# Kernel optimization log

Measured on AMD Instinct MI355X. Metric: run time of the kernel, lower is better.

Reference implementation:

```python
import jax, jax.numpy as jnp
import numpy as np

HEADS = 8
SCALE_BASE = 512
EPS = 1e-5


def xpos(x, downscale=False):
    # x: (B, h, S, hd) ; XPOS rotary embedding with exponential scale
    hd = x.shape[-1]
    S = x.shape[-2]
    half = hd // 2
    base_scale = (jnp.arange(0, hd, 2, dtype=jnp.float32) + 0.4 * hd) / (1.4 * hd)  # (half,)
    pos = jnp.arange(S, dtype=jnp.float32)
    scale = base_scale[None, :] ** (pos[:, None] / SCALE_BASE)  # (S, half)
    inv_freq = 1.0 / (10000.0 ** (jnp.arange(half, dtype=jnp.float32) / half))
    sinu = pos[:, None] * inv_freq[None, :]  # (S, half)
    sin, cos = jnp.sin(sinu), jnp.cos(sinu)
    if downscale:
        scale = 1.0 / scale
    # duplicate_interleave: (S, half) -> (S, hd)
    sin_s = jnp.repeat(sin * scale, 2, axis=-1)
    cos_s = jnp.repeat(cos * scale, 2, axis=-1)
    x1 = x[..., ::2]
    x2 = x[..., 1::2]
    rot = jnp.stack((-x2, x1), axis=-1).reshape(x.shape)  # rotate_every_two
    return x * cos_s + rot * sin_s


def decay_mask(S):
    # (heads, S, S): gamma^(n-m) for n>=m else 0
    gammas = 1.0 - jnp.exp(jnp.linspace(np.log(1 / 32), np.log(1 / 512), HEADS)).astype(jnp.float32)
    n = jnp.arange(S, dtype=jnp.float32)
    diff = n[:, None] - n[None, :]
    lg = jnp.log(gammas)[:, None, None]
    return jnp.where(diff >= 0, jnp.exp(jnp.maximum(diff, 0.0) * lg), 0.0)


def layer_norm(x, w, b):
    mu = x.mean(-1, keepdims=True)
    var = x.var(-1, keepdims=True)
    return (x - mu) / jnp.sqrt(var + EPS) * w + b


def multiscale_retention(Xq, Xkv, Wq, Wk, Wv, Wg, Wo, gn_w, gn_b):
    # Xq: (B,S,d) query source; Xkv: (B,S,d) key/value source (== Xq for self)
    B, S, _ = Xq.shape
    Q = jnp.einsum('bsd,hde->bhse', Xq, Wq)
    K = jnp.einsum('btd,hde->bhte', Xkv, Wk)
    V = jnp.einsum('btd,hdv->bhtv', Xkv, Wv)
    Q = xpos(Q)
    K = xpos(K, downscale=True)
    D = decay_mask(S)  # (h,S,S)
    scores = jnp.einsum('bhse,bhte->bhst', Q, K) * D[None]
    Y = jnp.einsum('bhst,bhtv->bhsv', scores, V)  # (B,h,S,hv)
    h, hv = Y.shape[1], Y.shape[3]
    # GroupNorm(heads, v_dim) over each head's channels per token
    mu = Y.mean(-1, keepdims=True)
    var = Y.var(-1, keepdims=True)
    Yn = (Y - mu) / jnp.sqrt(var + EPS)
    Yn = Yn.transpose(0, 2, 1, 3).reshape(B, S, h * hv) * gn_w + gn_b
    gate = jax.nn.sigmoid(Xq @ Wg) * (Xq @ Wg)  # swish gate
    return (gate * Yn) @ Wo


def setup_inputs() -> dict:
    key = jax.random.key(0)
    ks = jax.random.split(key, 32)
    d, f, h, hd, hv, vd = 1024, 4096, 8, 128, 256, 2048
    B, S = 2, 2048
    inp = {
        'X': jax.random.normal(ks[0], (B, S, d), jnp.float32),
        'mem': jax.random.normal(ks[1], (B, S, d), jnp.float32),
        'ln1_w': jax.random.uniform(ks[2], (d,), jnp.float32, 0.5, 1.5),
        'ln1_b': jax.random.normal(ks[3], (d,), jnp.float32) * 0.1,
        'ln2_w': jax.random.uniform(ks[4], (d,), jnp.float32, 0.5, 1.5),
        'ln2_b': jax.random.normal(ks[5], (d,), jnp.float32) * 0.1,
        'Wq': jax.random.normal(ks[6], (h, d, hd), jnp.float32) / d,
        'Wk': jax.random.normal(ks[7], (h, d, hd), jnp.float32) / d,
        'Wv': jax.random.normal(ks[8], (h, d, hv), jnp.float32) / d,
        'Wg': jax.random.normal(ks[9], (d, vd), jnp.float32) / d,
        'Wo': jax.random.normal(ks[10], (vd, d), jnp.float32) / d,
        'gn_w': jax.random.uniform(ks[11], (vd,), jnp.float32, 0.5, 1.5),
        'gn_b': jax.random.normal(ks[12], (vd,), jnp.float32) * 0.1,
        'cWq': jax.random.normal(ks[13], (h, d, hd), jnp.float32) / d,
        'cWk': jax.random.normal(ks[14], (h, d, hd), jnp.float32) / d,
        'cWv': jax.random.normal(ks[15], (h, d, hv), jnp.float32) / d,
        'cWg': jax.random.normal(ks[16], (d, vd), jnp.float32) / d,
        'cWo': jax.random.normal(ks[17], (vd, d), jnp.float32) / d,
        'cgn_w': jax.random.uniform(ks[18], (vd,), jnp.float32, 0.5, 1.5),
        'cgn_b': jax.random.normal(ks[19], (vd,), jnp.float32) * 0.1,
        'W1': jax.random.normal(ks[20], (d, f), jnp.float32) * (1.0 / np.sqrt(d)),
        'b1': jax.random.normal(ks[21], (f,), jnp.float32) * 0.02,
        'W2': jax.random.normal(ks[22], (f, d), jnp.float32) * (1.0 / np.sqrt(f)),
        'b2': jax.random.normal(ks[23], (d,), jnp.float32) * 0.02,
    }
    return inp


def reference(X, mem, ln1_w, ln1_b, ln2_w, ln2_b, Wq, Wk, Wv, Wg, Wo, gn_w, gn_b,
              cWq, cWk, cWv, cWg, cWo, cgn_w, cgn_b, W1, b1, W2, b2):
    # self retention block
    X = multiscale_retention(layer_norm(X, ln1_w, ln1_b), None, Wq, Wk, Wv, Wg, Wo, gn_w, gn_b) + X if False else multiscale_retention(layer_norm(X, ln1_w, ln1_b), layer_norm(X, ln1_w, ln1_b), Wq, Wk, Wv, Wg, Wo, gn_w, gn_b) + X
    # cross retention block (note: original reuses layer_norms_2 for both this and the FFN)
    h2 = layer_norm(X, ln2_w, ln2_b)
    X = multiscale_retention(h2, mem, cWq, cWk, cWv, cWg, cWo, cgn_w, cgn_b) + X
    # FFN block (GELU exact, per torch nn.GELU default)
    h3 = layer_norm(X, ln2_w, ln2_b)
    X = (jax.nn.gelu(h3 @ W1 + b1, approximate=False) @ W2 + b2) + X
    return X
```

## Files before the change

### kernel.cpp

```cpp
#include <hip/hip_runtime.h>
#include <math.h>

#define RTOT 4096
#define SEQQ 2048

typedef unsigned int uint32;
typedef __attribute__((ext_vector_type(4))) float f32x4;
typedef __attribute__((ext_vector_type(8))) short bf16x8;

__device__ __forceinline__ unsigned short f2bf(float f) {
  unsigned int u = __float_as_uint(f);
  u = (u + 0x7FFFu + ((u >> 16) & 1u)) >> 16;
  return (unsigned short)u;
}
__device__ __forceinline__ float bf2f(unsigned short h) {
  return __uint_as_float(((unsigned int)h) << 16);
}
__device__ __forceinline__ void gld16(const void* g, void* l) {
  __builtin_amdgcn_global_load_lds(
      (const __attribute__((address_space(1))) uint32*)g,
      (__attribute__((address_space(3))) uint32*)l, 16, 0, 0);
}
__device__ __forceinline__ void bar() {
  asm volatile("" ::: "memory");
  __builtin_amdgcn_s_barrier();
  asm volatile("" ::: "memory");
}
#define VMCNT(n) asm volatile("s_waitcnt vmcnt(" #n ")" ::: "memory")

__global__ __launch_bounds__(256) void transpose_bf16(
    const float* __restrict__ in, unsigned short* __restrict__ out, int R, int C,
    int perm) {
  __shared__ float t[32][33];
  int z = blockIdx.z;
  in  += (size_t)z * R * C;
  out += (size_t)z * C * R;
  int r0 = blockIdx.x * 32, c0 = blockIdx.y * 32;
  int tx = threadIdx.x & 31, ty = threadIdx.x >> 5;
  #pragma unroll
  for (int i = 0; i < 4; ++i) {
    int r = ty + i * 8;
    t[r][tx] = in[(size_t)(r0 + r) * C + c0 + tx];
  }
  __syncthreads();
  #pragma unroll
  for (int i = 0; i < 4; ++i) {
    int cc = c0 + ty + i * 8;
    if (perm) cc = 64 * (cc >> 6) + ((cc & 1) << 5) + ((cc & 63) >> 1);
    out[(size_t)cc * R + r0 + tx] = f2bf(t[tx][ty + i * 8]);
  }
}

__global__ __launch_bounds__(256) void cvt_bf16(
    const float* __restrict__ in, unsigned short* __restrict__ out, int n8) {
  int i = blockIdx.x * 256 + threadIdx.x;
  if (i >= n8) return;
  const float4* p = (const float4*)(in + (size_t)i * 8);
  float4 a = p[0], b = p[1];
  bf16x8 v;
  v[0] = (short)f2bf(a.x); v[1] = (short)f2bf(a.y); v[2] = (short)f2bf(a.z); v[3] = (short)f2bf(a.w);
  v[4] = (short)f2bf(b.x); v[5] = (short)f2bf(b.y); v[6] = (short)f2bf(b.z); v[7] = (short)f2bf(b.w);
  *(bf16x8*)(out + (size_t)i * 8) = v;
}

__global__ __launch_bounds__(256) void tabgen(float* __restrict__ tab) {
  int i = blockIdx.x * 256 + threadIdx.x;
  int pos = i >> 6, j = i & 63;
  float bs = (2.f * (float)j + 51.2f) * (1.f / 179.2f);
  float e = (float)pos * (1.f / 512.f);
  float sc = exp2f(e * log2f(bs));
  float invf = exp2f(-(float)j * (13.287712379549449f / 64.f));
  float su, cu;
  sincosf((float)pos * invf, &su, &cu);
  tab[i]            = cu * sc;
  tab[131072 + i]   = su * sc;
  float si = 1.f / sc;
  tab[262144 + i]   = cu * si;
  tab[393216 + i]   = su * si;
}

__global__ __launch_bounds__(256) void ln_bf16(const float* __restrict__ x,
    const float* __restrict__ w, const float* __restrict__ b,
    unsigned short* __restrict__ out) {
  int row = blockIdx.x, tid = threadIdx.x;
  const float* xr = x + (size_t)row * 1024;
  float4 v = *(const float4*)(xr + tid * 4);
  float s  = v.x + v.y + v.z + v.w;
  float ss = v.x*v.x + v.y*v.y + v.z*v.z + v.w*v.w;
  #pragma unroll
  for (int o = 32; o > 0; o >>= 1) { s += __shfl_down(s, o); ss += __shfl_down(ss, o); }
  __shared__ float red[2][4];
  int wid = tid >> 6;
  if ((tid & 63) == 0) { red[0][wid] = s; red[1][wid] = ss; }
  __syncthreads();
  float st  = red[0][0] + red[0][1] + red[0][2] + red[0][3];
  float sst = red[1][0] + red[1][1] + red[1][2] + red[1][3];
  float mu   = st * (1.f / 1024.f);
  float var  = sst * (1.f / 1024.f) - mu * mu;
  float rstd = rsqrtf(var + 1e-5f);
  float4 wv = *(const float4*)(w + tid * 4);
  float4 bv = *(const float4*)(b + tid * 4);
  unsigned short o0 = f2bf((v.x - mu) * rstd * wv.x + bv.x);
  unsigned short o1 = f2bf((v.y - mu) * rstd * wv.y + bv.y);
  unsigned short o2 = f2bf((v.z - mu) * rstd * wv.z + bv.z);
  unsigned short o3 = f2bf((v.w - mu) * rstd * wv.w + bv.w);
  ushort4 o4 = make_ushort4(o0, o1, o2, o3);
  *(ushort4*)(out + (size_t)row * 1024 + tid * 4) = o4;
}

enum { EPI_F32_RES = 0, EPI_BF16 = 1, EPI_XPOS = 2, EPI_GELU = 4, EPI_BRES = 5,
       EPI_QKG = 6, EPI_QG = 7 };

struct EpiP {
  void* C; int ldc;
  const float* bias; const float* resid;
  const float* tab;
  unsigned short* oQ; unsigned short* oK; unsigned short* oG;
};

template<int EPI>
__device__ __forceinline__ void epi_store(size_t m, int n, int N0, float v, const EpiP& P) {
  if constexpr (EPI == EPI_BF16) {
    ((unsigned short*)P.C)[m * P.ldc + n] = f2bf(v);
  } else if constexpr (EPI == EPI_GELU) {
    v += P.bias[n];
    v = 0.5f * v * (1.f + erff(v * 0.70710678f));
    ((unsigned short*)P.C)[m * P.ldc + n] = f2bf(v);
  } else if constexpr (EPI == EPI_BRES) {
    v += P.bias[n] + P.resid[m * P.ldc + n];
    ((float*)P.C)[m * P.ldc + n] = v;
  } else {
    v += P.resid[m * P.ldc + n];
    ((float*)P.C)[m * P.ldc + n] = v;
  }
}

template<int EPI>
__global__ __launch_bounds__(256) void gemm_mfma(
    const unsigned short* __restrict__ A, int lda,
    const unsigned short* __restrict__ Bt, int ldb, int K, EpiP P) {
  __shared__ __align__(16) unsigned short As[2][128 * 32];
  __shared__ __align__(16) unsigned short Bs[2][128 * 32];
  const int tid = threadIdx.x, w = tid >> 6, lane = tid & 63;
  const int M0 = blockIdx.y * 128, N0 = blockIdx.x * 128;
  const int fr = lane & 15, fs = lane >> 4;
  const int srow = lane >> 2, sp = lane & 3;

  f32x4 zf = {0.f, 0.f, 0.f, 0.f};
  f32x4 acc[4][4];
  #pragma unroll
  for (int i = 0; i < 4; ++i)
    #pragma unroll
    for (int j = 0; j < 4; ++j) acc[i][j] = zf;

  auto STAGE = [&](int buf, int k0) {
    #pragma unroll
    for (int c = 0; c < 4; ++c) {
      int ch = w * 4 + c;
      int cc = ch & 7;
      int row = cc * 16 + srow;
      int so = sp ^ ((row >> 1) & 3);
      if (ch < 8) gld16(A  + (size_t)(M0 + row) * lda + k0 + so * 8, &As[buf][cc * 512]);
      else        gld16(Bt + (size_t)(N0 + row) * ldb + k0 + so * 8, &Bs[buf][cc * 512]);
    }
  };

  STAGE(0, 0);
  int cur = 0;
  for (int k0 = 0; k0 < K; k0 += 32) {
    if (k0 + 32 < K) { STAGE(cur ^ 1, k0 + 32); VMCNT(4); }
    else             { VMCNT(0); }
    bar();
    bf16x8 af[4], bfr[4];
    #pragma unroll
    for (int mi = 0; mi < 4; ++mi) {
      int row = (w >> 1) * 64 + mi * 16 + fr;
      af[mi] = *(const bf16x8*)(&As[cur][row * 32 + (fs ^ ((row >> 1) & 3)) * 8]);
    }
    #pragma unroll
    for (int ni = 0; ni < 4; ++ni) {
      int row = (w & 1) * 64 + ni * 16 + fr;
      bfr[ni] = *(const bf16x8*)(&Bs[cur][row * 32 + (fs ^ ((row >> 1) & 3)) * 8]);
    }
    #pragma unroll
    for (int mi = 0; mi < 4; ++mi)
      #pragma unroll
      for (int ni = 0; ni < 4; ++ni)
        acc[mi][ni] = __builtin_amdgcn_mfma_f32_16x16x32_bf16(af[mi], bfr[ni], acc[mi][ni], 0, 0, 0);
    bar();
    cur ^= 1;
  }

  #pragma unroll
  for (int mi = 0; mi < 4; ++mi)
    #pragma unroll
    for (int r = 0; r < 4; ++r) {
      size_t m = M0 + (w >> 1) * 64 + mi * 16 + fs * 4 + r;
      #pragma unroll
      for (int ni = 0; ni < 4; ++ni) {
        int n = N0 + (w & 1) * 64 + ni * 16 + fr;
        epi_store<EPI>(m, n, N0, acc[mi][ni][r], P);
      }
    }
}

template<int EPI>
__global__ __launch_bounds__(256) void gemm_bn64(
    const unsigned short* __restrict__ A, int lda,
    const unsigned short* __restrict__ Bt, int ldb, int K, EpiP P) {
  __shared__ __align__(16) unsigned short As[2][128 * 32];
  __shared__ __align__(16) unsigned short Bs[2][64 * 32];
  const int tid = threadIdx.x, w = tid >> 6, lane = tid & 63;
  const int M0 = blockIdx.y * 128, N0 = blockIdx.x * 64;
  const int fr = lane & 15, fs = lane >> 4;
  const int srow = lane >> 2, sp = lane & 3;

  f32x4 zf = {0.f, 0.f, 0.f, 0.f};
  f32x4 acc[2][4];
  #pragma unroll
  for (int i = 0; i < 2; ++i)
    #pragma unroll
    for (int j = 0; j < 4; ++j) acc[i][j] = zf;

  auto STAGE = [&](int buf, int k0) {
    #pragma unroll
    for (int c = 0; c < 3; ++c) {
      int ch = w * 3 + c;
      if (ch < 8) {
        int row = ch * 16 + srow;
        int so = sp ^ ((row >> 1) & 3);
        gld16(A + (size_t)(M0 + row) * lda + k0 + so * 8, &As[buf][ch * 512]);
      } else {
        int bch = ch - 8;
        int row = bch * 16 + srow;
        int so = sp ^ ((row >> 1) & 3);
        gld16(Bt + (size_t)(N0 + row) * ldb + k0 + so * 8, &Bs[buf][bch * 512]);
      }
    }
  };

  STAGE(0, 0);
  int cur = 0;
  for (int k0 = 0; k0 < K; k0 += 32) {
    if (k0 + 32 < K) { STAGE(cur ^ 1, k0 + 32); VMCNT(3); }
    else             { VMCNT(0); }
    bar();
    bf16x8 af[2], bfr[4];
    #pragma unroll
    for (int mi = 0; mi < 2; ++mi) {
      int row = w * 32 + mi * 16 + fr;
      af[mi] = *(const bf16x8*)(&As[cur][row * 32 + (fs ^ ((row >> 1) & 3)) * 8]);
    }
    #pragma unroll
    for (int ni = 0; ni < 4; ++ni) {
      int row = ni * 16 + fr;
      bfr[ni] = *(const bf16x8*)(&Bs[cur][row * 32 + (fs ^ ((row >> 1) & 3)) * 8]);
    }
    #pragma unroll
    for (int mi = 0; mi < 2; ++mi)
      #pragma unroll
      for (int ni = 0; ni < 4; ++ni)
        acc[mi][ni] = __builtin_amdgcn_mfma_f32_16x16x32_bf16(af[mi], bfr[ni], acc[mi][ni], 0, 0, 0);
    bar();
    cur ^= 1;
  }

  if constexpr (EPI == EPI_XPOS) {
    int gsel = (N0 >> 6) & 1;
    #pragma unroll
    for (int mi = 0; mi < 2; ++mi)
      #pragma unroll
      for (int r = 0; r < 4; ++r) {
        size_t m = M0 + w * 32 + mi * 16 + fs * 4 + r;
        int pos = (int)(m & (SEQQ - 1));
        #pragma unroll
        for (int ni = 0; ni < 2; ++ni) {
          int j = gsel * 32 + ni * 16 + fr;
          float cs = P.tab[pos * 64 + j], sn = P.tab[131072 + pos * 64 + j];
          float ve = acc[mi][ni][r], vo = acc[mi][ni + 2][r];
          unsigned short* dst = (unsigned short*)P.C;
          dst[m * P.ldc + N0 + ni * 16 + fr]       = f2bf(ve * cs - vo * sn);
          dst[m * P.ldc + N0 + (ni + 2) * 16 + fr] = f2bf(vo * cs + ve * sn);
        }
      }
  } else {
    #pragma unroll
    for (int mi = 0; mi < 2; ++mi)
      #pragma unroll
      for (int r = 0; r < 4; ++r) {
        size_t m = M0 + w * 32 + mi * 16 + fs * 4 + r;
        #pragma unroll
        for (int ni = 0; ni < 4; ++ni) {
          int n = N0 + ni * 16 + fr;
          epi_store<EPI>(m, n, N0, acc[mi][ni][r], P);
        }
      }
  }
}

template<int EPI>
__global__ __launch_bounds__(512, 2) void gemm256(
    const unsigned short* __restrict__ A,
    const unsigned short* __restrict__ Bt,
    int nbx, EpiP P) {
  __shared__ __align__(16) unsigned short lds[4][2][8192];
  const int tid = threadIdx.x, w = tid >> 6, lane = tid & 63;
  int cpx = (int)gridDim.x >> 3;
  int sbid = ((int)blockIdx.x & 7) * cpx + ((int)blockIdx.x >> 3);
  int by = sbid / nbx, bx = sbid - by * nbx;
  const int M0 = by * 256, N0 = bx * 256;
  const int wm = w >> 2, wn = w & 3;
  const int fr = lane & 15, fs = lane >> 4;
  const int srow = lane >> 2;
  const int sslot = (lane & 3) ^ ((lane >> 3) & 3);
  const int rsw = (fr >> 1) & 3;

  f32x4 acc[8][4];
  #pragma unroll
  for (int i = 0; i < 8; ++i)
    #pragma unroll
    for (int j = 0; j < 4; ++j) acc[i][j] = {0.f, 0.f, 0.f, 0.f};

  auto STAGE = [&](int t, int buf) {
    int k0 = t * 32;
    #pragma unroll
    for (int j = 0; j < 4; ++j) {
      int c = w * 4 + j;
      if (c < 16)
        gld16(A  + (size_t)(M0 + c * 16 + srow) * 1024 + k0 + sslot * 8,
              &lds[buf][0][c * 512]);
      else
        gld16(Bt + (size_t)(N0 + (c - 16) * 16 + srow) * 1024 + k0 + sslot * 8,
              &lds[buf][1][(c - 16) * 512]);
    }
  };
  auto COMPUTE = [&](int t) {
    const unsigned short* la = &lds[t & 3][0][wm * 128 * 32];
    const unsigned short* lb = &lds[t & 3][1][wn * 64 * 32];
    bf16x8 a[8], b[4];
    #pragma unroll
    for (int ni = 0; ni < 4; ++ni)
      b[ni] = *(const bf16x8*)(lb + (ni * 16 + fr) * 32 + ((fs ^ rsw) * 8));
    #pragma unroll
    for (int mi = 0; mi < 8; ++mi)
      a[mi] = *(const bf16x8*)(la + (mi * 16 + fr) * 32 + ((fs ^ rsw) * 8));
    #pragma unroll
    for (int mi = 0; mi < 8; ++mi)
      #pragma unroll
      for (int ni = 0; ni < 4; ++ni)
        acc[mi][ni] = __builtin_amdgcn_mfma_f32_16x16x32_bf16(a[mi], b[ni], acc[mi][ni], 0, 0, 0);
  };

  STAGE(0, 0); STAGE(1, 1); STAGE(2, 2);
  for (int t = 0; t < 29; ++t) {
    STAGE(t + 3, (t + 3) & 3);
    VMCNT(12);
    bar();
    COMPUTE(t);
    bar();
  }
  VMCNT(8);  bar(); COMPUTE(29); bar();
  VMCNT(4);  bar(); COMPUTE(30); bar();
  VMCNT(0);  bar(); COMPUTE(31);

  if constexpr (EPI == EPI_GELU) {
    #pragma unroll
    for (int mi = 0; mi < 8; ++mi)
      #pragma unroll
      for (int r = 0; r < 4; ++r) {
        size_t m = M0 + wm * 128 + mi * 16 + fs * 4 + r;
        #pragma unroll
        for (int ni = 0; ni < 4; ++ni) {
          int n = N0 + wn * 64 + ni * 16 + fr;
          float v = acc[mi][ni][r] + P.bias[n];
          v = 0.5f * v * (1.f + erff(v * 0.70710678f));
          ((unsigned short*)P.C)[m * P.ldc + n] = f2bf(v);
        }
      }
  } else {
    const int nb = N0 + wn * 64;
    const bool isQ = nb < 1024;
    const bool isK = (EPI == EPI_QKG) && !isQ && (nb < 2048);
    if (isQ || isK) {
      const float* tc = isK ? P.tab + 262144 : P.tab;
      const float* ts = tc + 131072;
      unsigned short* dst = isK ? P.oK : P.oQ;
      const int nloc = isK ? nb - 1024 : nb;
      const int gsel = (nloc >> 6) & 1;
      #pragma unroll
      for (int mi = 0; mi < 8; ++mi)
        #pragma unroll
        for (int r = 0; r < 4; ++r) {
          size_t m = M0 + wm * 128 + mi * 16 + fs * 4 + r;
          int pos = (int)(m & (SEQQ - 1));
          #pragma unroll
          for (int ni = 0; ni < 2; ++ni) {
            int j = gsel * 32 + ni * 16 + fr;
            float cs = tc[pos * 64 + j], sn = ts[pos * 64 + j];
            float ve = acc[mi][ni][r], vo = acc[mi][ni + 2][r];
            dst[m * 1024 + nloc + ni * 16 + fr]       = f2bf(ve * cs - vo * sn);
            dst[m * 1024 + nloc + (ni + 2) * 16 + fr] = f2bf(vo * cs + ve * sn);
          }
        }
    } else {
      const int nloc = nb - ((EPI == EPI_QKG) ? 2048 : 1024);
      #pragma unroll
      for (int mi = 0; mi < 8; ++mi)
        #pragma unroll
        for (int r = 0; r < 4; ++r) {
          size_t m = M0 + wm * 128 + mi * 16 + fs * 4 + r;
          #pragma unroll
          for (int ni = 0; ni < 4; ++ni) {
            float v = acc[mi][ni][r];
            P.oG[m * 2048 + nloc + ni * 16 + fr] = f2bf(v / (1.f + expf(-v)));
          }
        }
    }
  }
}

__global__ __launch_bounds__(256) void retention_mfma(
    const unsigned short* __restrict__ Qx, const unsigned short* __restrict__ Kx,
    const unsigned short* __restrict__ VT, const unsigned short* __restrict__ Gate,
    const float* __restrict__ gnw, const float* __restrict__ gnb,
    unsigned short* __restrict__ Gout) {
  __shared__ __align__(16) unsigned short Ks[2][32 * 128];
  __shared__ __align__(16) unsigned short Vs[2][256 * 32];
  __shared__ __align__(16) float Ps[4][16 * 36];
  const int tid = threadIdx.x, w = tid >> 6, lane = tid & 63;
  int bid = blockIdx.x, qt, h, b;
  if (bid < 256) { qt = 31 - (bid >> 3); h = bid & 7; b = 0; }
  else           { int k = bid - 256; qt = k >> 3; h = k & 7; b = 1; }
  const int q0 = qt * 64;
  const int fr = lane & 15, fs = lane >> 4;

  float gamma = 1.f - expf(-3.4657359028f - 0.3960841032f * (float)h);
  float l2g = log2f(gamma);

  size_t qrow = (size_t)b * SEQQ + q0 + w * 16 + fr;
  bf16x8 qf[4];
  #pragma unroll
  for (int ks = 0; ks < 4; ++ks)
    qf[ks] = *(const bf16x8*)(Qx + qrow * 1024 + h * 128 + ks * 32 + fs * 8);

  float fqv[4];
  #pragma unroll
  for (int r = 0; r < 4; ++r)
    fqv[r] = exp2f((float)(q0 + w * 16 + fs * 4 + r) * l2g);

  f32x4 zf = {0.f, 0.f, 0.f, 0.f};
  f32x4 yacc[16];
  #pragma unroll
  for (int i = 0; i < 16; ++i) yacc[i] = zf;

  int cutoff = (int)(27.f / (-l2g));
  int t_start = q0 - cutoff;
  if (t_start < 0) t_start = 0;
  t_start &= ~31;
  size_t kbase = (size_t)b * SEQQ;

  auto STAGE = [&](int buf, int t0) {
    #pragma unroll
    for (int c = 0; c < 2; ++c) {
      int ch = w * 2 + c;
      int row = ch * 4 + (lane >> 4);
      int so = (lane & 15) ^ (row & 15);
      gld16(Kx + (kbase + t0 + row) * 1024 + h * 128 + so * 8, &Ks[buf][ch * 512]);
    }
    #pragma unroll
    for (int c = 0; c < 4; ++c) {
      int ch = w * 4 + c;
      int vrow = ch * 16 + (lane >> 2);
      int so = (lane & 3) ^ ((vrow >> 1) & 3);
      gld16(VT + (size_t)(h * 256 + vrow) * RTOT + kbase + t0 + so * 8, &Vs[buf][ch * 512]);
    }
  };

  STAGE(0, t_start);
  int cur = 0;
  for (int t0 = t_start; t0 < q0 + 64; t0 += 32) {
    if (t0 + 32 < q0 + 64) { STAGE(cur ^ 1, t0 + 32); VMCNT(6); }
    else                   { VMCNT(0); }
    bar();

    f32x4 sacc[2];
    sacc[0] = zf; sacc[1] = zf;
    #pragma unroll
    for (int nt = 0; nt < 2; ++nt) {
      int row = nt * 16 + fr;
      #pragma unroll
      for (int ks = 0; ks < 4; ++ks) {
        int sl = ks * 4 + fs;
        bf16x8 kf = *(const bf16x8*)(&Ks[cur][row * 128 + (sl ^ (row & 15)) * 8]);
        sacc[nt] = __builtin_amdgcn_mfma_f32_16x16x32_bf16(qf[ks], kf, sacc[nt], 0, 0, 0);
      }
    }
    float ftv[2];
    ftv[0] = exp2f((float)(t0 + fr)      * -l2g);
    ftv[1] = exp2f((float)(t0 + 16 + fr) * -l2g);
    float* Pw = Ps[w];
    #pragma unroll
    for (int nt = 0; nt < 2; ++nt) {
      #pragma unroll
      for (int r = 0; r < 4; ++r) {
        int sl_ = fs * 4 + r;
        int diff = (q0 + w * 16 + sl_) - (t0 + nt * 16 + fr);
        float v = (diff >= 0) ? sacc[nt][r] * (fqv[r] * ftv[nt]) : 0.f;
        Pw[sl_ * 36 + nt * 16 + fr] = v;
      }
    }
    f32x4 pa = *(const f32x4*)(Pw + fr * 36 + fs * 8);
    f32x4 pb = *(const f32x4*)(Pw + fr * 36 + fs * 8 + 4);
    bf16x8 pf;
    pf[0] = (short)f2bf(pa[0]); pf[1] = (short)f2bf(pa[1]);
    pf[2] = (short)f2bf(pa[2]); pf[3] = (short)f2bf(pa[3]);
    pf[4] = (short)f2bf(pb[0]); pf[5] = (short)f2bf(pb[1]);
    pf[6] = (short)f2bf(pb[2]); pf[7] = (short)f2bf(pb[3]);
    #pragma unroll
    for (int nv = 0; nv < 16; ++nv) {
      int vrow = nv * 16 + fr;
      bf16x8 vf = *(const bf16x8*)(&Vs[cur][vrow * 32 + (fs ^ ((vrow >> 1) & 3)) * 8]);
      yacc[nv] = __builtin_amdgcn_mfma_f32_16x16x32_bf16(pf, vf, yacc[nv], 0, 0, 0);
    }
    bar();
    cur ^= 1;
  }

  #pragma unroll
  for (int r = 0; r < 4; ++r) {
    float s = 0.f, sq = 0.f;
    #pragma unroll
    for (int nv = 0; nv < 16; ++nv) { float v = yacc[nv][r]; s += v; sq += v * v; }
    #pragma unroll
    for (int msk = 1; msk < 16; msk <<= 1) { s += __shfl_xor(s, msk); sq += __shfl_xor(sq, msk); }
    float mu = s * (1.f / 256.f);
    float var = sq * (1.f / 256.f) - mu * mu;
    float rstd = rsqrtf(var + 1e-5f);
    int srow = q0 + w * 16 + fs * 4 + r;
    size_t mrow = (size_t)b * SEQQ + srow;
    const unsigned short* grow = Gate + mrow * 2048 + h * 256;
    unsigned short* orow = Gout + mrow * 2048 + h * 256;
    #pragma unroll
    for (int nv = 0; nv < 16; ++nv) {
      int col = nv * 16 + fr;
      float yn = (yacc[nv][r] - mu) * rstd * gnw[h * 256 + col] + gnb[h * 256 + col];
      orow[col] = f2bf(bf2f(grow[col]) * yn);
    }
  }
}

extern "C" void kernel_launch(void* const* d_in, const int* in_sizes, int n_in,
                              void* d_out, int out_size, void* d_ws, size_t ws_size,
                              hipStream_t stream) {
  const float* X    = (const float*)d_in[0];
  const float* mem  = (const float*)d_in[1];
  const float* ln1w = (const float*)d_in[2];
  const float* ln1b = (const float*)d_in[3];
  const float* ln2w = (const float*)d_in[4];
  const float* ln2b = (const float*)d_in[5];
  const float* Wq   = (const float*)d_in[6];
  const float* Wk   = (const float*)d_in[7];
  const float* Wv   = (const float*)d_in[8];
  const float* Wg   = (const float*)d_in[9];
  const float* Wo   = (const float*)d_in[10];
  const float* gnw  = (const float*)d_in[11];
  const float* gnb  = (const float*)d_in[12];
  const float* cWq  = (const float*)d_in[13];
  const float* cWk  = (const float*)d_in[14];
  const float* cWv  = (const float*)d_in[15];
  const float* cWg  = (const float*)d_in[16];
  const float* cWo  = (const float*)d_in[17];
  const float* cgnw = (const float*)d_in[18];
  const float* cgnb = (const float*)d_in[19];
  const float* W1   = (const float*)d_in[20];
  const float* b1   = (const float*)d_in[21];
  const float* W2   = (const float*)d_in[22];
  const float* b2   = (const float*)d_in[23];
  float* out = (float*)d_out;

  const size_t MB = 1024ull * 1024ull;
  if (ws_size < 106 * MB) return;
  unsigned char* W8 = (unsigned char*)d_ws;
  unsigned short* WqkgT = (unsigned short*)(W8 + 0 * MB);
  unsigned short* WvT   = (unsigned short*)(W8 + 8 * MB);
  unsigned short* WoT   = (unsigned short*)(W8 + 12 * MB);
  unsigned short* cQGT  = (unsigned short*)(W8 + 16 * MB);
  unsigned short* cWkT  = (unsigned short*)(W8 + 22 * MB);
  unsigned short* cWvT  = (unsigned short*)(W8 + 24 * MB);
  unsigned short* cWoT  = (unsigned short*)(W8 + 28 * MB);
  float*          tab   = (float*)(W8 + 32 * MB);
  unsigned short* hbuf  = (unsigned short*)(W8 + 34 * MB);
  unsigned short* Qx    = (unsigned short*)(W8 + 42 * MB);
  unsigned short* Kx    = (unsigned short*)(W8 + 50 * MB);
  unsigned short* W1T   = Qx;
  unsigned short* W2T   = Kx;
  unsigned short* VTb   = (unsigned short*)(W8 + 58 * MB);
  unsigned short* Gg    = (unsigned short*)(W8 + 74 * MB);
  unsigned short* Tb    = VTb;
  unsigned short* GoutB = (unsigned short*)(W8 + 90 * MB);
  unsigned short* mem16 = GoutB;

  transpose_bf16<<<dim3(32, 4, 8),  256, 0, stream>>>(Wq,  WqkgT,               1024, 128, 1);
  transpose_bf16<<<dim3(32, 4, 8),  256, 0, stream>>>(Wk,  WqkgT + 1024 * 1024, 1024, 128, 1);
  transpose_bf16<<<dim3(32, 64, 1), 256, 0, stream>>>(Wg,  WqkgT + 2048 * 1024, 1024, 2048, 0);
  transpose_bf16<<<dim3(32, 8, 8),  256, 0, stream>>>(Wv,  WvT,  1024, 256, 0);
  transpose_bf16<<<dim3(64, 32, 1), 256, 0, stream>>>(Wo,  WoT,  2048, 1024, 0);
  transpose_bf16<<<dim3(32, 4, 8),  256, 0, stream>>>(cWq, cQGT,               1024, 128, 1);
  transpose_bf16<<<dim3(32, 64, 1), 256, 0, stream>>>(cWg, cQGT + 1024 * 1024, 1024, 2048, 0);
  transpose_bf16<<<dim3(32, 4, 8),  256, 0, stream>>>(cWk, cWkT, 1024, 128, 1);
  transpose_bf16<<<dim3(32, 8, 8),  256, 0, stream>>>(cWv, cWvT, 1024, 256, 0);
  transpose_bf16<<<dim3(64, 32, 1), 256, 0, stream>>>(cWo, cWoT, 2048, 1024, 0);
  tabgen<<<512, 256, 0, stream>>>(tab);

  EpiP P{};

  ln_bf16<<<RTOT, 256, 0, stream>>>(X, ln1w, ln1b, hbuf);
  P = EpiP{nullptr, 0, nullptr, nullptr, tab, Qx, Kx, Gg};
  gemm256<EPI_QKG><<<256, 512, 0, stream>>>(hbuf, WqkgT, 16, P);
  P = EpiP{VTb, 4096, nullptr, nullptr, nullptr, nullptr, nullptr, nullptr};
  gemm_mfma<EPI_BF16><<<dim3(32, 16), 256, 0, stream>>>(WvT, 1024, hbuf, 1024, 1024, P);
  retention_mfma<<<dim3(512), 256, 0, stream>>>(Qx, Kx, VTb, Gg, gnw, gnb, GoutB);
  P = EpiP{out, 1024, nullptr, X, nullptr, nullptr, nullptr, nullptr};
  gemm_bn64<EPI_F32_RES><<<dim3(16, 32), 256, 0, stream>>>(GoutB, 2048, WoT, 2048, 2048, P);

  cvt_bf16<<<2048, 256, 0, stream>>>(mem, mem16, 524288);
  ln_bf16<<<RTOT, 256, 0, stream>>>(out, ln2w, ln2b, hbuf);
  P = EpiP{nullptr, 0, nullptr, nullptr, tab, Qx, nullptr, Gg};
  gemm256<EPI_QG><<<192, 512, 0, stream>>>(hbuf, cQGT, 12, P);
  P = EpiP{Kx, 1024, nullptr, nullptr, tab + 262144, nullptr, nullptr, nullptr};
  gemm_bn64<EPI_XPOS><<<dim3(16, 32), 256, 0, stream>>>(mem16, 1024, cWkT, 1024, 1024, P);
  P = EpiP{VTb, 4096, nullptr, nullptr, nullptr, nullptr, nullptr, nullptr};
  gemm_mfma<EPI_BF16><<<dim3(32, 16), 256, 0, stream>>>(cWvT, 1024, mem16, 1024, 1024, P);
  retention_mfma<<<dim3(512), 256, 0, stream>>>(Qx, Kx, VTb, Gg, cgnw, cgnb, GoutB);
  P = EpiP{out, 1024, nullptr, out, nullptr, nullptr, nullptr, nullptr};
  gemm_bn64<EPI_F32_RES><<<dim3(16, 32), 256, 0, stream>>>(GoutB, 2048, cWoT, 2048, 2048, P);

  transpose_bf16<<<dim3(32, 128, 1), 256, 0, stream>>>(W1, W1T, 1024, 4096, 0);
  transpose_bf16<<<dim3(128, 32, 1), 256, 0, stream>>>(W2, W2T, 4096, 1024, 0);
  ln_bf16<<<RTOT, 256, 0, stream>>>(out, ln2w, ln2b, hbuf);
  P = EpiP{Tb, 4096, b1, nullptr, nullptr, nullptr, nullptr, nullptr};
  gemm256<EPI_GELU><<<256, 512, 0, stream>>>(hbuf, W1T, 16, P);
  P = EpiP{out, 1024, b2, out, nullptr, nullptr, nullptr, nullptr};
  gemm_bn64<EPI_BRES><<<dim3(16, 32), 256, 0, stream>>>(Tb, 4096, W2T, 4096, 4096, P);
}
```

Baseline: 588.3 us.

## Triple-buffer GEMM k-loop and move retention P fragments through shuffles instead of LDS

Both GEMM kernels go from double to triple buffering of the A/B LDS tiles, prefetching two k-steps ahead with adjusted vmcnt waits, so more load latency is hidden. In the retention kernel the QK^T MFMA operands are swapped to produce the transposed score layout. The decay mask is computed as one exp2 per tile times precomputed per-lane factors, and the P fragment is packed to bf16 and redistributed with cross-lane shuffles rather than a round trip through shared memory. In exchange the GEMMs use more LDS, which can lower occupancy, and the retention path issues extra shuffle instructions.

```diff
diff --git a/kernel.cpp b/kernel.cpp
--- a/kernel.cpp
+++ b/kernel.cpp
@@ -139,8 +139,8 @@
 __global__ __launch_bounds__(256) void gemm_mfma(
     const unsigned short* __restrict__ A, int lda,
     const unsigned short* __restrict__ Bt, int ldb, int K, EpiP P) {
-  __shared__ __align__(16) unsigned short As[2][128 * 32];
-  __shared__ __align__(16) unsigned short Bs[2][128 * 32];
+  __shared__ __align__(16) unsigned short As[3][128 * 32];
+  __shared__ __align__(16) unsigned short Bs[3][128 * 32];
   const int tid = threadIdx.x, w = tid >> 6, lane = tid & 63;
   const int M0 = blockIdx.y * 128, N0 = blockIdx.x * 128;
   const int fr = lane & 15, fs = lane >> 4;
@@ -165,11 +165,14 @@
     }
   };
 
+  const int NT = K >> 5;
   STAGE(0, 0);
-  int cur = 0;
-  for (int k0 = 0; k0 < K; k0 += 32) {
-    if (k0 + 32 < K) { STAGE(cur ^ 1, k0 + 32); VMCNT(4); }
-    else             { VMCNT(0); }
+  STAGE(1, 32);
+  int cur = 0, sb = 1;
+  for (int t = 0; t < NT; ++t) {
+    if (t + 2 < NT)      { sb = (sb == 2) ? 0 : sb + 1; STAGE(sb, (t + 2) * 32); VMCNT(8); }
+    else if (t + 1 < NT) { VMCNT(4); }
+    else                 { VMCNT(0); }
     bar();
     bf16x8 af[4], bfr[4];
     #pragma unroll
@@ -188,7 +191,7 @@
       for (int ni = 0; ni < 4; ++ni)
         acc[mi][ni] = __builtin_amdgcn_mfma_f32_16x16x32_bf16(af[mi], bfr[ni], acc[mi][ni], 0, 0, 0);
     bar();
-    cur ^= 1;
+    cur = (cur == 2) ? 0 : cur + 1;
   }
 
   #pragma unroll
@@ -208,8 +211,8 @@
 __global__ __launch_bounds__(256) void gemm_bn64(
     const unsigned short* __restrict__ A, int lda,
     const unsigned short* __restrict__ Bt, int ldb, int K, EpiP P) {
-  __shared__ __align__(16) unsigned short As[2][128 * 32];
-  __shared__ __align__(16) unsigned short Bs[2][64 * 32];
+  __shared__ __align__(16) unsigned short As[3][128 * 32];
+  __shared__ __align__(16) unsigned short Bs[3][64 * 32];
   const int tid = threadIdx.x, w = tid >> 6, lane = tid & 63;
   const int M0 = blockIdx.y * 128, N0 = blockIdx.x * 64;
   const int fr = lane & 15, fs = lane >> 4;
@@ -239,11 +242,14 @@
     }
   };
 
+  const int NT = K >> 5;
   STAGE(0, 0);
-  int cur = 0;
-  for (int k0 = 0; k0 < K; k0 += 32) {
-    if (k0 + 32 < K) { STAGE(cur ^ 1, k0 + 32); VMCNT(3); }
-    else             { VMCNT(0); }
+  STAGE(1, 32);
+  int cur = 0, sb = 1;
+  for (int t = 0; t < NT; ++t) {
+    if (t + 2 < NT)      { sb = (sb == 2) ? 0 : sb + 1; STAGE(sb, (t + 2) * 32); VMCNT(6); }
+    else if (t + 1 < NT) { VMCNT(3); }
+    else                 { VMCNT(0); }
     bar();
     bf16x8 af[2], bfr[4];
     #pragma unroll
@@ -262,7 +268,7 @@
       for (int ni = 0; ni < 4; ++ni)
         acc[mi][ni] = __builtin_amdgcn_mfma_f32_16x16x32_bf16(af[mi], bfr[ni], acc[mi][ni], 0, 0, 0);
     bar();
-    cur ^= 1;
+    cur = (cur == 2) ? 0 : cur + 1;
   }
 
   if constexpr (EPI == EPI_XPOS) {
@@ -426,7 +432,6 @@
     unsigned short* __restrict__ Gout) {
   __shared__ __align__(16) unsigned short Ks[2][32 * 128];
   __shared__ __align__(16) unsigned short Vs[2][256 * 32];
-  __shared__ __align__(16) float Ps[4][16 * 36];
   const int tid = threadIdx.x, w = tid >> 6, lane = tid & 63;
   int bid = blockIdx.x, qt, h, b;
   if (bid < 256) { qt = 31 - (bid >> 3); h = bid & 7; b = 0; }
@@ -436,17 +441,20 @@
 
   float gamma = 1.f - expf(-3.4657359028f - 0.3960841032f * (float)h);
   float l2g = log2f(gamma);
-
-  size_t qrow = (size_t)b * SEQQ + q0 + w * 16 + fr;
+  const int qglob = q0 + w * 16 + fr;
+
+  size_t qrow = (size_t)b * SEQQ + qglob;
   bf16x8 qf[4];
   #pragma unroll
   for (int ks = 0; ks < 4; ++ks)
     qf[ks] = *(const bf16x8*)(Qx + qrow * 1024 + h * 128 + ks * 32 + fs * 8);
 
-  float fqv[4];
-  #pragma unroll
-  for (int r = 0; r < 4; ++r)
-    fqv[r] = exp2f((float)(q0 + w * 16 + fs * 4 + r) * l2g);
+  float gtl8[8];
+  #pragma unroll
+  for (int i = 0; i < 8; ++i) {
+    int toff = (i >> 2) * 16 + fs * 4 + (i & 3);
+    gtl8[i] = exp2f(-(float)toff * l2g);
+  }
 
   f32x4 zf = {0.f, 0.f, 0.f, 0.f};
   f32x4 yacc[16];
@@ -492,35 +500,34 @@
       for (int ks = 0; ks < 4; ++ks) {
         int sl = ks * 4 + fs;
         bf16x8 kf = *(const bf16x8*)(&Ks[cur][row * 128 + (sl ^ (row & 15)) * 8]);
-        sacc[nt] = __builtin_amdgcn_mfma_f32_16x16x32_bf16(qf[ks], kf, sacc[nt], 0, 0, 0);
+        sacc[nt] = __builtin_amdgcn_mfma_f32_16x16x32_bf16(kf, qf[ks], sacc[nt], 0, 0, 0);
       }
     }
-    float ftv[2];
-    ftv[0] = exp2f((float)(t0 + fr)      * -l2g);
-    ftv[1] = exp2f((float)(t0 + 16 + fr) * -l2g);
-    float* Pw = Ps[w];
-    #pragma unroll
-    for (int nt = 0; nt < 2; ++nt) {
-      #pragma unroll
-      for (int r = 0; r < 4; ++r) {
-        int sl_ = fs * 4 + r;
-        int diff = (q0 + w * 16 + sl_) - (t0 + nt * 16 + fr);
-        float v = (diff >= 0) ? sacc[nt][r] * (fqv[r] * ftv[nt]) : 0.f;
-        Pw[sl_ * 36 + nt * 16 + fr] = v;
+    float fsc = exp2f((float)(qglob - t0) * l2g);
+    uint32 pk[4];
+    #pragma unroll
+    for (int nt = 0; nt < 2; ++nt)
+      #pragma unroll
+      for (int hf = 0; hf < 2; ++hf) {
+        int r0i = hf * 2;
+        int ta = t0 + nt * 16 + fs * 4 + r0i;
+        float va = (qglob >= ta)     ? sacc[nt][r0i]     * (fsc * gtl8[nt * 4 + r0i])     : 0.f;
+        float vb = (qglob >= ta + 1) ? sacc[nt][r0i + 1] * (fsc * gtl8[nt * 4 + r0i + 1]) : 0.f;
+        pk[nt * 2 + hf] = (uint32)f2bf(va) | ((uint32)f2bf(vb) << 16);
       }
-    }
-    f32x4 pa = *(const f32x4*)(Pw + fr * 36 + fs * 8);
-    f32x4 pb = *(const f32x4*)(Pw + fr * 36 + fs * 8 + 4);
-    bf16x8 pf;
-    pf[0] = (short)f2bf(pa[0]); pf[1] = (short)f2bf(pa[1]);
-    pf[2] = (short)f2bf(pa[2]); pf[3] = (short)f2bf(pa[3]);
-    pf[4] = (short)f2bf(pb[0]); pf[5] = (short)f2bf(pb[1]);
-    pf[6] = (short)f2bf(pb[2]); pf[7] = (short)f2bf(pb[3]);
+    union { uint32 u[4]; bf16x8 v8; } pa;
+    #pragma unroll
+    for (int j = 0; j < 4; ++j) {
+      int src = fr + 16 * (2 * (fs & 1) + (j >> 1));
+      int v0 = __shfl((int)pk[j & 1],     src);
+      int v1 = __shfl((int)pk[2 + (j & 1)], src);
+      pa.u[j] = (fs < 2) ? (uint32)v0 : (uint32)v1;
+    }
     #pragma unroll
     for (int nv = 0; nv < 16; ++nv) {
       int vrow = nv * 16 + fr;
       bf16x8 vf = *(const bf16x8*)(&Vs[cur][vrow * 32 + (fs ^ ((vrow >> 1) & 3)) * 8]);
-      yacc[nv] = __builtin_amdgcn_mfma_f32_16x16x32_bf16(pf, vf, yacc[nv], 0, 0, 0);
+      yacc[nv] = __builtin_amdgcn_mfma_f32_16x16x32_bf16(pa.v8, vf, yacc[nv], 0, 0, 0);
     }
     bar();
     cur ^= 1;
```

Result: no change. 589.1 us (+0.1%).
